# Kernel optimization log

Measured on AMD Instinct MI355X. Metric: run time of the kernel, lower is better.

The kernel has to match this reference:

```python
import jax, jax.numpy as jnp
import numpy as np

B, C, N, M = 4, 192, 160, 160
HEADS, DH = 4, 32
HID = HEADS * DH
NMEM = 4
SCALE = DH ** -0.5


def setup_inputs() -> dict:
    key = jax.random.key(0)
    ks = jax.random.split(key, 8)
    std = 0.05
    return {
        "x": jax.random.normal(ks[0], (B, C, N, M), jnp.float32),
        "gq": jnp.ones((C,), jnp.float32),
        "gk": jnp.ones((C,), jnp.float32),
        "gv": jnp.ones((C,), jnp.float32),
        "Wq": jax.random.normal(ks[1], (HID, C), jnp.float32) * std,
        "Wk": jax.random.normal(ks[2], (HID, C), jnp.float32) * std,
        "Wv": jax.random.normal(ks[3], (HID, C), jnp.float32) * std,
        "mem_kv": jax.random.normal(ks[4], (2, HEADS, NMEM, DH), jnp.float32),
        "Wo": jax.random.normal(ks[5], (C, HID), jnp.float32) * std,
        "bo": jnp.zeros((C,), jnp.float32),
        "Wr": jax.random.normal(ks[6], (C, 2 * C), jnp.float32) * std,
    }


def _rms(x, g):
    # lucidrains RMSNorm over channel axis 1: F.normalize(x, dim=1) * g * sqrt(dim)
    n = jnp.sqrt(jnp.sum(x * x, axis=1, keepdims=True))
    gshape = (1, -1) + (1,) * (x.ndim - 2)
    return x / jnp.maximum(n, 1e-12) * g.reshape(gshape) * jnp.sqrt(jnp.asarray(x.shape[1], x.dtype))


def _axial_attn(q_ft, k_ft, v_map, rep, Wq, Wk, Wv, mem_kv, Wo, bo, gq, gk, gv):
    # q_ft: (b, c, Lq) compact queries (spatial (1,Lq) in the original)
    # k_ft: (b, c, Lk) compact keys; original repeats them `rep` times -> (Lk*rep) keys
    # v_map: (b, c, Lk, rep) values (full map, not broadcast)
    # Exact math of softmax over [NMEM + Lk*rep] keys, exploiting the rep-fold
    # duplicated key scores so attn(key i, copy j) has identical weight p_i:
    #   out = sum_mem p_j mem_v_j + sum_i p_i * (sum_rep v[i, r])
    b = q_ft.shape[0]
    q = jnp.einsum('hdc,bcq->bhqd', Wq.reshape(HEADS, DH, -1), _rms(q_ft, gq))
    k = jnp.einsum('hdc,bck->bhkd', Wk.reshape(HEADS, DH, -1), _rms(k_ft, gk))
    v = jnp.einsum('hdc,bckr->bhkrd', Wv.reshape(HEADS, DH, -1), _rms(v_map, gv))
    v_sum = v.sum(axis=3)  # (b,h,Lk,d)
    mem_k, mem_v = mem_kv[0], mem_kv[1]
    s_k = jnp.einsum('bhqd,bhkd->bhqk', q, k) * SCALE      # (b,h,Lq,Lk)
    s_m = jnp.einsum('bhqd,hjd->bhqj', q, mem_k) * SCALE   # (b,h,Lq,NMEM)
    mx = jnp.maximum(s_k.max(-1), s_m.max(-1))             # (b,h,Lq)
    e_k = jnp.exp(s_k - mx[..., None])
    e_m = jnp.exp(s_m - mx[..., None])
    Z = e_m.sum(-1) + rep * e_k.sum(-1)                    # rep copies of each key
    out = (jnp.einsum('bhqj,hjd->bhqd', e_m, mem_v)
           + jnp.einsum('bhqk,bhkd->bhqd', e_k, v_sum)) / Z[..., None]
    out = out.transpose(0, 2, 1, 3).reshape(b, -1, HID)    # (b,Lq,hid), (h d) channel order
    return jnp.einsum('ck,bqk->bcq', Wo, out) + bo[None, :, None]  # (b,c,Lq)


def reference(x, gq, gk, gv, Wq, Wk, Wv, mem_kv, Wo, bo, Wr):
    # x: (b,c,n,m); mask=None path
    row_ft = x.mean(axis=3)  # (b,c,n)
    col_ft = x.mean(axis=2)  # (b,c,m)
    # row attention: n queries, keys = col_ft repeated n times, values = x^T (spatial (m,n))
    row_attn = _axial_attn(row_ft, col_ft, x.transpose(0, 1, 3, 2), N,
                           Wq, Wk, Wv, mem_kv, Wo, bo, gq, gk, gv)  # (b,c,n)
    # col attention (shared weights): m queries, keys = row_ft repeated m times, values = x
    col_attn = _axial_attn(col_ft, row_ft, x, M,
                           Wq, Wk, Wv, mem_kv, Wo, bo, gq, gk, gv)  # (b,c,m)
    # broadcast to (b,c,n,m), concat on channels, 1x1 conv reduce (bias=False)
    Wr1, Wr2 = Wr[:, :C], Wr[:, C:]
    out = (jnp.einsum('dc,bcn->bdn', Wr1, row_attn)[:, :, :, None]
           + jnp.einsum('dc,bcm->bdm', Wr2, col_attn)[:, :, None, :])
    return out
```

## Files before the change

kernel.cpp:

```cpp
#include <hip/hip_runtime.h>
#include <math.h>

constexpr int B_ = 4, C_ = 192, N_ = 160, M_ = 160;
constexpr int NM_ = N_ * M_;
constexpr float SQRT_C = 13.856406460551018f;
constexpr float SCALE_ = 0.17677669529663687f;

__device__ __forceinline__ float wred_sum(float v) {
    #pragma unroll
    for (int o = 32; o > 0; o >>= 1) v += __shfl_xor(v, o, 64);
    return v;
}
__device__ __forceinline__ float wred_max(float v) {
    #pragma unroll
    for (int o = 32; o > 0; o >>= 1) v = fmaxf(v, __shfl_xor(v, o, 64));
    return v;
}

__global__ __launch_bounds__(256) void mega1_kernel(
        const float* __restrict__ x,
        const float* __restrict__ Wr, const float* __restrict__ Wo,
        const float* __restrict__ bo,
        const float* __restrict__ Wq, const float* __restrict__ Wk,
        const float* __restrict__ Wv, const float* __restrict__ gq,
        const float* __restrict__ gk, const float* __restrict__ gv,
        float* __restrict__ psum,
        float* __restrict__ rowft, float* __restrict__ colft,
        float* __restrict__ WfT2, float* __restrict__ bfb,
        float* __restrict__ WT) {
    __shared__ float cpart[4][160];
    int bx = blockIdx.x, tid = threadIdx.x;
    if (bx < 2400) {
        int chunk = bx / 400, blk = bx % 400;
        int g = blk * 256 + tid;
        int b = g / NM_, nm = g - b * NM_;
        const float* xp = x + ((size_t)(b * C_ + chunk * 32)) * NM_ + nm;
        float ssq = 0.f;
        #pragma unroll
        for (int cc = 0; cc < 32; cc++) { float v = xp[(size_t)cc * NM_]; ssq += v * v; }
        psum[chunk * (B_ * NM_) + g] = ssq;
    } else if (bx < 3168) {
        int bc = bx - 2400;
        int w = tid >> 6, lane = tid & 63;
        const float* xp = x + (size_t)bc * NM_;
        int m0 = lane, m1 = lane + 64, m2 = lane + 128;
        bool ok2 = (m2 < M_);
        float cr0 = 0.f, cr1 = 0.f, cr2 = 0.f;
        for (int n = w; n < N_; n += 4) {
            const float* xr = xp + n * M_;
            float a0 = xr[m0], a1 = xr[m1], a2 = ok2 ? xr[m2] : 0.f;
            cr0 += a0; cr1 += a1; cr2 += a2;
            float rs = wred_sum(a0 + a1 + a2);
            if (lane == 0) rowft[bc * N_ + n] = rs * (1.0f / 160.0f);
        }
        cpart[w][m0] = cr0; cpart[w][m1] = cr1; if (ok2) cpart[w][m2] = cr2;
        __syncthreads();
        if (tid < M_) {
            float sr = 0.f;
            #pragma unroll
            for (int ww = 0; ww < 4; ww++) sr += cpart[ww][tid];
            colft[bc * M_ + tid] = sr * (1.0f / 160.0f);
        }
    } else if (bx < 3360) {
        int pair = (bx - 3168) * 2 + (tid >> 7);
        int hd = tid & 127;
        int t = pair / 192, dch = pair % 192;
        const float* wr = Wr + dch * 384 + t * 192;
        float acc = 0.f;
        for (int c = 0; c < 192; c++) acc += wr[c] * Wo[c * 128 + hd];
        WfT2[pair * 128 + hd] = acc;
        if (hd == 0) {
            float sb = 0.f;
            for (int c = 0; c < 192; c++) sb += wr[c] * bo[c];
            bfb[pair] = sb;
        }
    } else {
        int g = (bx - 3360) * 256 + tid;
        int mat = g / 24576, r2 = g - mat * 24576;
        const float* W  = (mat == 0) ? Wq : ((mat == 1) ? Wk : Wv);
        const float* gp = (mat == 0) ? gq : ((mat == 1) ? gk : gv);
        WT[g] = gp[r2 % 192] * W[r2];
    }
}

__global__ __launch_bounds__(256) void rnorm_kernel(
        const float* __restrict__ psum, float* __restrict__ rn) {
    int g = blockIdx.x * 256 + threadIdx.x;
    float s = 0.f;
    #pragma unroll
    for (int ch = 0; ch < 6; ch++) s += psum[ch * (B_ * NM_) + g];
    rn[g] = SQRT_C / fmaxf(sqrtf(s), 1e-12f);
}

__global__ __launch_bounds__(512) void sweighted_kernel(
        const float* __restrict__ x, const float* __restrict__ rn,
        float* __restrict__ Srow, float* __restrict__ Scol) {
    __shared__ float cpart[8][160];
    int bc = blockIdx.x;
    int b = bc / C_;
    int tid = threadIdx.x, w = tid >> 6, lane = tid & 63;
    const float* xp = x + (size_t)bc * NM_;
    const float* rp = rn + (size_t)b * NM_;
    int m0 = lane, m1 = lane + 64, m2 = lane + 128;
    bool ok2 = (m2 < M_);
    float cn0 = 0.f, cn1 = 0.f, cn2 = 0.f;
    for (int n = w; n < N_; n += 8) {
        const float* xr = xp + n * M_;
        const float* rr = rp + n * M_;
        float b0 = xr[m0] * rr[m0];
        float b1 = xr[m1] * rr[m1];
        float b2 = ok2 ? xr[m2] * rr[m2] : 0.f;
        cn0 += b0; cn1 += b1; cn2 += b2;
        float rsn = wred_sum(b0 + b1 + b2);
        if (lane == 0) Srow[bc * N_ + n] = rsn;
    }
    cpart[w][m0] = cn0; cpart[w][m1] = cn1; if (ok2) cpart[w][m2] = cn2;
    __syncthreads();
    if (tid < M_) {
        float sn = 0.f;
        #pragma unroll
        for (int ww = 0; ww < 8; ww++) sn += cpart[ww][tid];
        Scol[bc * M_ + tid] = sn;
    }
}

__global__ __launch_bounds__(256) void proj_kernel(
        const float* __restrict__ WT,
        const float* __restrict__ rowft, const float* __restrict__ colft,
        const float* __restrict__ Srow, const float* __restrict__ Scol,
        float* __restrict__ Qb, float* __restrict__ Kb, float* __restrict__ Vb) {
    __shared__ float in_s[4 * 196];
    __shared__ float sc_s[4];
    int bx = blockIdx.x;
    int pt = bx % 40, rest = bx / 40;
    int mat = rest % 3; int r2 = rest / 3;
    int t = r2 % 2, b = r2 / 2;
    const float* src; float* dst;
    if (mat == 0)      { src = (t == 0) ? rowft : colft; dst = Qb; }
    else if (mat == 1) { src = (t == 0) ? colft : rowft; dst = Kb; }
    else               { src = (t == 0) ? Scol  : Srow;  dst = Vb; }
    const float* Wt = WT + mat * 24576;
    int tid = threadIdx.x;
    for (int idx = tid; idx < 768; idx += 256) {
        int c = idx >> 2, p = idx & 3;
        in_s[p * 196 + c] = src[(b * C_ + c) * 160 + pt * 4 + p];
    }
    __syncthreads();
    int w = tid >> 6, lane = tid & 63;
    if (mat < 2) {
        float v0 = in_s[w * 196 + lane];
        float v1 = in_s[w * 196 + lane + 64];
        float v2 = in_s[w * 196 + lane + 128];
        float ssq = wred_sum(v0 * v0 + v1 * v1 + v2 * v2);
        if (lane == 0) sc_s[w] = SQRT_C / fmaxf(sqrtf(ssq), 1e-12f);
    } else {
        if (tid < 4) sc_s[tid] = 1.0f;
    }
    __syncthreads();
    int hd = tid & 127, p0 = (tid >> 7) * 2;
    const float* wp = Wt + hd * 192;
    const float* i0p = &in_s[p0 * 196];
    const float* i1p = &in_s[(p0 + 1) * 196];
    float a0 = 0.f, a1 = 0.f;
    #pragma unroll 4
    for (int c0 = 0; c0 < 192; c0 += 4) {
        float4 wv = *reinterpret_cast<const float4*>(wp + c0);
        float4 u0 = *reinterpret_cast<const float4*>(i0p + c0);
        float4 u1 = *reinterpret_cast<const float4*>(i1p + c0);
        a0 += wv.x * u0.x + wv.y * u0.y + wv.z * u0.z + wv.w * u0.w;
        a1 += wv.x * u1.x + wv.y * u1.y + wv.z * u1.z + wv.w * u1.w;
    }
    int posbase = (b * 2 + t) * 160 + pt * 4 + p0;
    dst[(size_t)posbase * 128 + hd]       = a0 * sc_s[p0];
    dst[(size_t)(posbase + 1) * 128 + hd] = a1 * sc_s[p0 + 1];
}

__global__ __launch_bounds__(256) void attn_kernel(
        const float* __restrict__ Qb, const float* __restrict__ Kb,
        const float* __restrict__ Vb, const float* __restrict__ memkv,
        float* __restrict__ AO) {
    __shared__ float k_s[160 * 36];
    __shared__ float v_s[32 * 172];
    __shared__ float q_s[8 * 36];
    __shared__ float e_s[8 * 160];
    __shared__ float mk[128];
    __shared__ float mv[128];
    int bx = blockIdx.x;
    int qt = bx % 20; int r = bx / 20;
    int h = r & 3; r >>= 2;
    int t = r & 1; int b = r >> 1;
    int tid = threadIdx.x, w = tid >> 6, lane = tid & 63;
    int btbase = ((b * 2 + t) * 160) * 128 + h * 32;
    for (int idx = tid; idx < 1280; idx += 256) {
        int k = idx >> 3, dq = idx & 7;
        float4 kv = *reinterpret_cast<const float4*>(Kb + btbase + k * 128 + dq * 4);
        *reinterpret_cast<float4*>(&k_s[k * 36 + dq * 4]) = kv;
        float4 vv = *reinterpret_cast<const float4*>(Vb + btbase + k * 128 + dq * 4);
        v_s[(dq * 4 + 0) * 172 + k] = vv.x;
        v_s[(dq * 4 + 1) * 172 + k] = vv.y;
        v_s[(dq * 4 + 2) * 172 + k] = vv.z;
        v_s[(dq * 4 + 3) * 172 + k] = vv.w;
    }
    if (tid < 64) {
        int q = tid >> 3, dq = tid & 7;
        *reinterpret_cast<float4*>(&q_s[q * 36 + dq * 4]) =
            *reinterpret_cast<const float4*>(Qb + btbase + (qt * 8 + q) * 128 + dq * 4);
    }
    if (tid < 128) {
        mk[tid] = memkv[h * 128 + tid];
        mv[tid] = memkv[512 + h * 128 + tid];
    }
    __syncthreads();
    float4 kr0[8], kr1[8], kr2[8];
    #pragma unroll
    for (int dq = 0; dq < 8; dq++) {
        kr0[dq] = *reinterpret_cast<const float4*>(&k_s[lane * 36 + dq * 4]);
        kr1[dq] = *reinterpret_cast<const float4*>(&k_s[(lane + 64) * 36 + dq * 4]);
        if (lane < 32) kr2[dq] = *reinterpret_cast<const float4*>(&k_s[(lane + 128) * 36 + dq * 4]);
        else           kr2[dq] = make_float4(0.f, 0.f, 0.f, 0.f);
    }
    float p;
    {
        int pj = lane >> 3, qi = pj >> 2, j = pj & 3;
        int db = (lane & 7) * 4;
        float4 qv = *reinterpret_cast<const float4*>(&q_s[(w * 2 + qi) * 36 + db]);
        float4 mkv = *reinterpret_cast<const float4*>(&mk[j * 32 + db]);
        p = qv.x * mkv.x + qv.y * mkv.y + qv.z * mkv.z + qv.w * mkv.w;
        p += __shfl_xor(p, 1, 64); p += __shfl_xor(p, 2, 64); p += __shfl_xor(p, 4, 64);
        p *= SCALE_;
    }
    float sm[2][4];
    #pragma unroll
    for (int j = 0; j < 4; j++) {
        sm[0][j] = __shfl(p, j * 8, 64);
        sm[1][j] = __shfl(p, 32 + j * 8, 64);
    }
    int dpv = lane & 31;
    float Zq[2], accm[2];
    #pragma unroll
    for (int qi = 0; qi < 2; qi++) {
        const float* qrow = &q_s[(w * 2 + qi) * 36];
        float s0 = 0.f, s1 = 0.f, s2 = 0.f;
        #pragma unroll
        for (int dq = 0; dq < 8; dq++) {
            float4 qv = *reinterpret_cast<const float4*>(qrow + dq * 4);
            s0 += qv.x * kr0[dq].x + qv.y * kr0[dq].y + qv.z * kr0[dq].z + qv.w * kr0[dq].w;
            s1 += qv.x * kr1[dq].x + qv.y * kr1[dq].y + qv.z * kr1[dq].z + qv.w * kr1[dq].w;
            s2 += qv.x * kr2[dq].x + qv.y * kr2[dq].y + qv.z * kr2[dq].z + qv.w * kr2[dq].w;
        }
        s0 *= SCALE_; s1 *= SCALE_;
        s2 = (lane < 32) ? s2 * SCALE_ : -1e30f;
        float mx = fmaxf(fmaxf(s0, s1), s2);
        mx = fmaxf(mx, fmaxf(fmaxf(sm[qi][0], sm[qi][1]), fmaxf(sm[qi][2], sm[qi][3])));
        mx = wred_max(mx);
        float e0 = __expf(s0 - mx), e1 = __expf(s1 - mx);
        float e2 = (lane < 32) ? __expf(s2 - mx) : 0.f;
        int eb = (w * 2 + qi) * 160;
        e_s[eb + lane] = e0; e_s[eb + 64 + lane] = e1;
        if (lane < 32) e_s[eb + 128 + lane] = e2;
        float esum = wred_sum(e0 + e1 + e2);
        float em0 = __expf(sm[qi][0] - mx), em1 = __expf(sm[qi][1] - mx);
        float em2 = __expf(sm[qi][2] - mx), em3 = __expf(sm[qi][3] - mx);
        Zq[qi] = (em0 + em1 + em2 + em3) + 160.0f * esum;
        accm[qi] = em0 * mv[dpv] + em1 * mv[32 + dpv] + em2 * mv[64 + dpv] + em3 * mv[96 + dpv];
    }
    int half = lane >> 5, k0 = half * 80;
    const float* vrow = &v_s[dpv * 172 + k0];
    const float* e0p = &e_s[(w * 2) * 160 + k0];
    const float* e1p = &e_s[(w * 2 + 1) * 160 + k0];
    float a0 = 0.f, a1 = 0.f;
    #pragma unroll 4
    for (int kk = 0; kk < 80; kk += 4) {
        float4 vv = *reinterpret_cast<const float4*>(vrow + kk);
        float4 e0 = *reinterpret_cast<const float4*>(e0p + kk);
        float4 e1 = *reinterpret_cast<const float4*>(e1p + kk);
        a0 += e0.x * vv.x + e0.y * vv.y + e0.z * vv.z + e0.w * vv.w;
        a1 += e1.x * vv.x + e1.y * vv.y + e1.z * vv.z + e1.w * vv.w;
    }
    a0 += __shfl_down(a0, 32, 64);
    a1 += __shfl_down(a1, 32, 64);
    if (lane < 32) {
        AO[btbase + (qt * 8 + w * 2 + 0) * 128 + lane] = (accm[0] + a0) / Zq[0];
        AO[btbase + (qt * 8 + w * 2 + 1) * 128 + lane] = (accm[1] + a1) / Zq[1];
    }
}

__global__ __launch_bounds__(192) void oproj_kernel(
        const float* __restrict__ WfT2, const float* __restrict__ bfb,
        const float* __restrict__ AO, float* __restrict__ Rr,
        float* __restrict__ Ccv) {
    __shared__ float ao_s[2 * 128];
    int bx = blockIdx.x;
    int pt = bx % 80, rest = bx / 80;
    int t = rest & 1, b = rest >> 1;
    int tid = threadIdx.x;
    for (int idx = tid; idx < 256; idx += 192)
        ao_s[idx] = AO[(size_t)((b * 2 + t) * 160 + pt * 2 + (idx >> 7)) * 128 + (idx & 127)];
    __syncthreads();
    int tofs = t * 192 + tid;
    const float* wp = WfT2 + tofs * 128;
    float a0 = 0.f, a1 = 0.f;
    #pragma unroll 8
    for (int hd = 0; hd < 128; hd += 4) {
        float4 w4 = *reinterpret_cast<const float4*>(wp + hd);
        float4 x0 = *reinterpret_cast<const float4*>(&ao_s[hd]);
        float4 x1 = *reinterpret_cast<const float4*>(&ao_s[128 + hd]);
        a0 += w4.x * x0.x + w4.y * x0.y + w4.z * x0.z + w4.w * x0.w;
        a1 += w4.x * x1.x + w4.y * x1.y + w4.z * x1.z + w4.w * x1.w;
    }
    float bb = bfb[tofs];
    float* dst = t ? Ccv : Rr;
    dst[(b * C_ + tid) * 160 + pt * 2 + 0] = a0 + bb;
    dst[(b * C_ + tid) * 160 + pt * 2 + 1] = a1 + bb;
}

__global__ __launch_bounds__(256) void final_kernel(
        const float* __restrict__ Rr, const float* __restrict__ Ccv,
        float* __restrict__ out) {
    __shared__ float Rl[160];
    __shared__ float Cl[160];
    int bd = blockIdx.x;
    int tid = threadIdx.x;
    if (tid < 160) { Rl[tid] = Rr[bd * 160 + tid]; Cl[tid] = Ccv[bd * 160 + tid]; }
    __syncthreads();
    float* base = out + (size_t)bd * NM_;
    for (int idx = tid; idx < 160 * 40; idx += 256) {
        int n = idx / 40, m4 = idx - n * 40;
        float r = Rl[n];
        float4 v;
        v.x = r + Cl[m4 * 4 + 0];
        v.y = r + Cl[m4 * 4 + 1];
        v.z = r + Cl[m4 * 4 + 2];
        v.w = r + Cl[m4 * 4 + 3];
        *reinterpret_cast<float4*>(base + n * 160 + m4 * 4) = v;
    }
}

extern "C" void kernel_launch(void* const* d_in, const int* in_sizes, int n_in,
                              void* d_out, int out_size, void* d_ws, size_t ws_size,
                              hipStream_t stream) {
    const float* x    = (const float*)d_in[0];
    const float* gq   = (const float*)d_in[1];
    const float* gk   = (const float*)d_in[2];
    const float* gv   = (const float*)d_in[3];
    const float* Wq   = (const float*)d_in[4];
    const float* Wk   = (const float*)d_in[5];
    const float* Wv   = (const float*)d_in[6];
    const float* mkv  = (const float*)d_in[7];
    const float* Wo   = (const float*)d_in[8];
    const float* bo   = (const float*)d_in[9];
    const float* Wr   = (const float*)d_in[10];
    float* out = (float*)d_out;

    float* ws = (float*)d_ws;
    float* rn    = ws;
    float* rowft = rn    + 102400;
    float* colft = rowft + 122880;
    float* Srow  = colft + 122880;
    float* Scol  = Srow  + 122880;
    float* WT    = Scol  + 122880;
    float* Qb    = WT    + 73728;
    float* Kb    = Qb    + 163840;
    float* Vb    = Kb    + 163840;
    float* AO    = Vb    + 163840;
    float* Rr    = AO    + 163840;
    float* Ccv   = Rr    + 122880;
    float* WfT   = Ccv   + 122880;
    float* bfb   = WfT   + 49152;
    float* psum  = Qb;

    mega1_kernel<<<3648, 256, 0, stream>>>(x, Wr, Wo, bo, Wq, Wk, Wv, gq, gk, gv,
                                           psum, rowft, colft, WfT, bfb, WT);
    rnorm_kernel<<<400, 256, 0, stream>>>(psum, rn);
    sweighted_kernel<<<768, 512, 0, stream>>>(x, rn, Srow, Scol);
    proj_kernel<<<960, 256, 0, stream>>>(WT, rowft, colft, Srow, Scol, Qb, Kb, Vb);
    attn_kernel<<<640, 256, 0, stream>>>(Qb, Kb, Vb, mkv, AO);
    oproj_kernel<<<640, 192, 0, stream>>>(WfT, bfb, AO, Rr, Ccv);
    final_kernel<<<768, 256, 0, stream>>>(Rr, Ccv, out);
}
```

Baseline: 242.7 us.

## Fuse channel-norm reduction into mega kernel and vectorize x reads with float4

The sum-of-squares pass now splits the 192 channels across the 4 waves of a block and reduces them in shared memory, writing the reciprocal norm directly. This removes the separate rnorm kernel and the psum scratch round-trip. The row/column mean and weighted-sum kernels switch to float4 loads over 40 lanes per row, so 24 lanes per wave sit idle. The sum-of-squares part runs on far fewer blocks (400 instead of 2400), with longer per-thread loops, which may lower parallelism while the whole x tensor is read.

```diff
diff --git a/kernel.cpp b/kernel.cpp
--- a/kernel.cpp
+++ b/kernel.cpp
@@ -24,45 +24,59 @@
         const float* __restrict__ Wq, const float* __restrict__ Wk,
         const float* __restrict__ Wv, const float* __restrict__ gq,
         const float* __restrict__ gk, const float* __restrict__ gv,
-        float* __restrict__ psum,
+        float* __restrict__ rn,
         float* __restrict__ rowft, float* __restrict__ colft,
         float* __restrict__ WfT2, float* __restrict__ bfb,
         float* __restrict__ WT) {
+    __shared__ float4 sp4[4][64];
     __shared__ float cpart[4][160];
     int bx = blockIdx.x, tid = threadIdx.x;
-    if (bx < 2400) {
-        int chunk = bx / 400, blk = bx % 400;
-        int g = blk * 256 + tid;
-        int b = g / NM_, nm = g - b * NM_;
-        const float* xp = x + ((size_t)(b * C_ + chunk * 32)) * NM_ + nm;
-        float ssq = 0.f;
-        #pragma unroll
-        for (int cc = 0; cc < 32; cc++) { float v = xp[(size_t)cc * NM_]; ssq += v * v; }
-        psum[chunk * (B_ * NM_) + g] = ssq;
-    } else if (bx < 3168) {
-        int bc = bx - 2400;
-        int w = tid >> 6, lane = tid & 63;
+    int w = tid >> 6, lane = tid & 63;
+    if (bx < 400) {
+        int g4 = bx * 64 + lane;
+        int b = g4 / 6400, nm4 = g4 - b * 6400;
+        const float* xb = x + (size_t)b * (C_ * NM_) + (size_t)nm4 * 4
+                            + (size_t)(w * 48) * NM_;
+        float4 s = make_float4(0.f, 0.f, 0.f, 0.f);
+        #pragma unroll 16
+        for (int cc = 0; cc < 48; cc++) {
+            float4 v = *reinterpret_cast<const float4*>(xb + (size_t)cc * NM_);
+            s.x += v.x * v.x; s.y += v.y * v.y; s.z += v.z * v.z; s.w += v.w * v.w;
+        }
+        sp4[w][lane] = s;
+        __syncthreads();
+        if (tid < 64) {
+            float4 a = sp4[0][tid], b2 = sp4[1][tid], c2 = sp4[2][tid], d2 = sp4[3][tid];
+            float4 r;
+            r.x = SQRT_C / fmaxf(sqrtf(a.x + b2.x + c2.x + d2.x), 1e-12f);
+            r.y = SQRT_C / fmaxf(sqrtf(a.y + b2.y + c2.y + d2.y), 1e-12f);
+            r.z = SQRT_C / fmaxf(sqrtf(a.z + b2.z + c2.z + d2.z), 1e-12f);
+            r.w = SQRT_C / fmaxf(sqrtf(a.w + b2.w + c2.w + d2.w), 1e-12f);
+            *reinterpret_cast<float4*>(rn + (size_t)(bx * 64 + tid) * 4) = r;
+        }
+    } else if (bx < 1168) {
+        int bc = bx - 400;
         const float* xp = x + (size_t)bc * NM_;
-        int m0 = lane, m1 = lane + 64, m2 = lane + 128;
-        bool ok2 = (m2 < M_);
-        float cr0 = 0.f, cr1 = 0.f, cr2 = 0.f;
+        bool act = (lane < 40);
+        float4 cs = make_float4(0.f, 0.f, 0.f, 0.f);
         for (int n = w; n < N_; n += 4) {
-            const float* xr = xp + n * M_;
-            float a0 = xr[m0], a1 = xr[m1], a2 = ok2 ? xr[m2] : 0.f;
-            cr0 += a0; cr1 += a1; cr2 += a2;
-            float rs = wred_sum(a0 + a1 + a2);
+            float4 v = act ? *reinterpret_cast<const float4*>(xp + n * M_ + lane * 4)
+                           : make_float4(0.f, 0.f, 0.f, 0.f);
+            cs.x += v.x; cs.y += v.y; cs.z += v.z; cs.w += v.w;
+            float rs = wred_sum(v.x + v.y + v.z + v.w);
             if (lane == 0) rowft[bc * N_ + n] = rs * (1.0f / 160.0f);
         }
-        cpart[w][m0] = cr0; cpart[w][m1] = cr1; if (ok2) cpart[w][m2] = cr2;
+        if (act) {
+            cpart[w][lane * 4 + 0] = cs.x; cpart[w][lane * 4 + 1] = cs.y;
+            cpart[w][lane * 4 + 2] = cs.z; cpart[w][lane * 4 + 3] = cs.w;
+        }
         __syncthreads();
-        if (tid < M_) {
-            float sr = 0.f;
-            #pragma unroll
-            for (int ww = 0; ww < 4; ww++) sr += cpart[ww][tid];
+        if (tid < 160) {
+            float sr = cpart[0][tid] + cpart[1][tid] + cpart[2][tid] + cpart[3][tid];
             colft[bc * M_ + tid] = sr * (1.0f / 160.0f);
         }
-    } else if (bx < 3360) {
-        int pair = (bx - 3168) * 2 + (tid >> 7);
+    } else if (bx < 1360) {
+        int pair = (bx - 1168) * 2 + (tid >> 7);
         int hd = tid & 127;
         int t = pair / 192, dch = pair % 192;
         const float* wr = Wr + dch * 384 + t * 192;
@@ -75,21 +89,12 @@
             bfb[pair] = sb;
         }
     } else {
-        int g = (bx - 3360) * 256 + tid;
+        int g = (bx - 1360) * 256 + tid;
         int mat = g / 24576, r2 = g - mat * 24576;
         const float* W  = (mat == 0) ? Wq : ((mat == 1) ? Wk : Wv);
         const float* gp = (mat == 0) ? gq : ((mat == 1) ? gk : gv);
         WT[g] = gp[r2 % 192] * W[r2];
     }
-}
-
-__global__ __launch_bounds__(256) void rnorm_kernel(
-        const float* __restrict__ psum, float* __restrict__ rn) {
-    int g = blockIdx.x * 256 + threadIdx.x;
-    float s = 0.f;
-    #pragma unroll
-    for (int ch = 0; ch < 6; ch++) s += psum[ch * (B_ * NM_) + g];
-    rn[g] = SQRT_C / fmaxf(sqrtf(s), 1e-12f);
 }
 
 __global__ __launch_bounds__(512) void sweighted_kernel(
@@ -101,22 +106,25 @@
     int tid = threadIdx.x, w = tid >> 6, lane = tid & 63;
     const float* xp = x + (size_t)bc * NM_;
     const float* rp = rn + (size_t)b * NM_;
-    int m0 = lane, m1 = lane + 64, m2 = lane + 128;
-    bool ok2 = (m2 < M_);
-    float cn0 = 0.f, cn1 = 0.f, cn2 = 0.f;
+    bool act = (lane < 40);
+    float4 acc = make_float4(0.f, 0.f, 0.f, 0.f);
     for (int n = w; n < N_; n += 8) {
-        const float* xr = xp + n * M_;
-        const float* rr = rp + n * M_;
-        float b0 = xr[m0] * rr[m0];
-        float b1 = xr[m1] * rr[m1];
-        float b2 = ok2 ? xr[m2] * rr[m2] : 0.f;
-        cn0 += b0; cn1 += b1; cn2 += b2;
-        float rsn = wred_sum(b0 + b1 + b2);
-        if (lane == 0) Srow[bc * N_ + n] = rsn;
-    }
-    cpart[w][m0] = cn0; cpart[w][m1] = cn1; if (ok2) cpart[w][m2] = cn2;
-    __syncthreads();
-    if (tid < M_) {
+        float4 xv = act ? *reinterpret_cast<const float4*>(xp + n * M_ + lane * 4)
+                        : make_float4(0.f, 0.f, 0.f, 0.f);
+        float4 rv = act ? *reinterpret_cast<const float4*>(rp + n * M_ + lane * 4)
+                        : make_float4(0.f, 0.f, 0.f, 0.f);
+        float4 p;
+        p.x = xv.x * rv.x; p.y = xv.y * rv.y; p.z = xv.z * rv.z; p.w = xv.w * rv.w;
+        acc.x += p.x; acc.y += p.y; acc.z += p.z; acc.w += p.w;
+        float rs = wred_sum(p.x + p.y + p.z + p.w);
+        if (lane == 0) Srow[bc * N_ + n] = rs;
+    }
+    if (act) {
+        cpart[w][lane * 4 + 0] = acc.x; cpart[w][lane * 4 + 1] = acc.y;
+        cpart[w][lane * 4 + 2] = acc.z; cpart[w][lane * 4 + 3] = acc.w;
+    }
+    __syncthreads();
+    if (tid < 160) {
         float sn = 0.f;
         #pragma unroll
         for (int ww = 0; ww < 8; ww++) sn += cpart[ww][tid];
@@ -367,11 +375,9 @@
     float* Ccv   = Rr    + 122880;
     float* WfT   = Ccv   + 122880;
     float* bfb   = WfT   + 49152;
-    float* psum  = Qb;
-
-    mega1_kernel<<<3648, 256, 0, stream>>>(x, Wr, Wo, bo, Wq, Wk, Wv, gq, gk, gv,
-                                           psum, rowft, colft, WfT, bfb, WT);
-    rnorm_kernel<<<400, 256, 0, stream>>>(psum, rn);
+
+    mega1_kernel<<<1648, 256, 0, stream>>>(x, Wr, Wo, bo, Wq, Wk, Wv, gq, gk, gv,
+                                           rn, rowft, colft, WfT, bfb, WT);
     sweighted_kernel<<<768, 512, 0, stream>>>(x, rn, Srow, Scol);
     proj_kernel<<<960, 256, 0, stream>>>(WT, rowft, colft, Srow, Scol, Qb, Kb, Vb);
     attn_kernel<<<640, 256, 0, stream>>>(Qb, Kb, Vb, mkv, AO);
```

New measurement: 240.2 us. About the same (-1.0%).
